# Kernel optimization log

Hardware: AMD Instinct MI355X
Metric: run time of the kernel (lower is better)

The kernel has to match this reference:

```python
import jax, jax.numpy as jnp
from jax import lax
import numpy as np

T, N, C, D, K = 256, 4096, 12, 256, 12


def setup_inputs() -> dict:
    key = jax.random.key(0)
    ks = jax.random.split(key, 11)
    g = lambda k, shape: (jax.random.normal(k, shape, jnp.float32) * 0.05)
    return {
        "x": jax.random.normal(ks[0], (T, N, C), jnp.float32),
        "enc_Wx": g(ks[1], (D, C)),
        "enc_bx": g(ks[2], (D,)),
        "enc_Wh": g(ks[3], (D, D)),
        "enc_Wy": g(ks[4], (K, D)),
        "enc_by": g(ks[5], (K,)),
        "dec_Wx": g(ks[6], (D, C)),
        "dec_bx": g(ks[7], (D,)),
        "dec_Wh": g(ks[8], (D, D)),
        "dec_Wy": g(ks[9], (K, D)),
        "dec_by": g(ks[10], (K,)),
    }


def reference(x, enc_Wx, enc_bx, enc_Wh, enc_Wy, enc_by,
              dec_Wx, dec_bx, dec_Wh, dec_Wy, dec_by):
    # x: (T, N, C)
    Tn, Nn, Cn = x.shape
    Dn = enc_Wh.shape[0]

    # ---- encoder Elman RNN: h_t = relu(x2h(x_t) + h2h(h_{t-1})) ----
    # Precompute input projection for all timesteps (batched GEMM),
    # leaving only the D x D recurrence inside the scan.
    x_proj = jnp.einsum('tnc,dc->tnd', x, enc_Wx) + enc_bx  # (T, N, D)

    def enc_step(h, xp):
        h = jax.nn.relu(xp + h @ enc_Wh.T)
        return h, None

    h0 = jnp.zeros((Nn, Dn), x.dtype)
    h_last, _ = lax.scan(enc_step, h0, x_proj)  # (N, D) == enc_h[-1]
    # (encoder h2y output is computed in the original but discarded)

    # ---- decoder: greedy feedback loop, T steps ----
    sos0 = jnp.zeros((Nn, Cn), x.dtype).at[:, -2].set(1.0)

    def dec_step(carry, _):
        h, sos = carry
        h = jax.nn.relu(sos @ dec_Wx.T + dec_bx + h @ dec_Wh.T)  # (N, D)
        y = h @ dec_Wy.T + dec_by                                # (N, K)
        sos = jax.nn.one_hot(jnp.argmax(y, axis=-1), y.shape[-1],
                             dtype=x.dtype)                      # (N, C)
        return (h, sos), y

    _, ys = lax.scan(dec_step, (h_last, sos0), None, length=Tn)
    return ys  # (T, N, K)
```

## Files before the change

### kernel.cpp

```cpp
#include <hip/hip_runtime.h>
#include <cstdint>
#include <cstddef>

#define TT 256
#define NN 4096
#define CC 12
#define DD 256
#define KD 12
#define NB 16
#define NTH 512
#define HS 264
#define XS 40

typedef _Float16 half8 __attribute__((ext_vector_type(8)));
typedef float f32x4 __attribute__((ext_vector_type(4)));
#define MFMA __builtin_amdgcn_mfma_f32_16x16x32_f16

struct FalseC { static constexpr bool value = false; };
struct TrueC  { static constexpr bool value = true;  };

struct alignas(16) SM {
  _Float16 hhi[2][NB][HS];
  _Float16 hlo[2][NB][HS];
  _Float16 xhi[4][NB][XS];
  _Float16 xlo[4][NB][XS];
  float    part[8][64][4];
  int      idxbuf[16];
};

__device__ __forceinline__ void split8(const float* w, half8& hi, half8& lo) {
  #pragma unroll
  for (int j = 0; j < 8; ++j) {
    _Float16 h = (_Float16)w[j];
    hi[j] = h;
    lo[j] = (_Float16)(w[j] - (float)h);
  }
}

__device__ __forceinline__ void BAR() {
  asm volatile("s_waitcnt lgkmcnt(0)" ::: "memory");
  __builtin_amdgcn_s_barrier();
  __builtin_amdgcn_sched_barrier(0);
}

__global__ __launch_bounds__(NTH, 2)
void seq2seq_kernel(const float* __restrict__ x,
                    const float* __restrict__ enc_Wx,
                    const float* __restrict__ enc_bx,
                    const float* __restrict__ enc_Wh,
                    const float* __restrict__ dec_Wx,
                    const float* __restrict__ dec_bx,
                    const float* __restrict__ dec_Wh,
                    const float* __restrict__ dec_Wy,
                    const float* __restrict__ dec_by,
                    float* __restrict__ out)
{
  __shared__ SM sm;
  const int tid  = (int)threadIdx.x;
  const int wid  = tid >> 6;
  const int lane = tid & 63;
  const int l15  = lane & 15;
  const int quad = lane >> 4;
  const int n0   = (int)blockIdx.x * NB;

  half8 Whi[2][8], Wlo[2][8];
  half8 Xhi[2], Xlo[2];
  float bxr[2];
  float pfA0 = 0.f, pfA1 = 0.f, pfA2 = 0.f;
  float pfB0 = 0.f, pfB1 = 0.f, pfB2 = 0.f;

  if (wid == 1) {
    const float* xg = x + ((size_t)1 * NN + n0) * CC;
    pfB0 = xg[lane]; pfB1 = xg[lane + 64]; pfB2 = xg[lane + 128];
  }

  auto loadWh = [&](const float* __restrict__ W) {
    #pragma unroll
    for (int tt = 0; tt < 2; ++tt) {
      const int n = (wid * 2 + tt) * 16 + l15;
      #pragma unroll
      for (int c = 0; c < 8; ++c) {
        float w[8];
        const float* p = W + (size_t)n * DD + c * 32 + quad * 8;
        *(float4*)&w[0] = *(const float4*)p;
        *(float4*)&w[4] = *(const float4*)(p + 4);
        split8(w, Whi[tt][c], Wlo[tt][c]);
      }
    }
  };
  auto loadWx = [&](const float* __restrict__ Wx) {
    #pragma unroll
    for (int tt = 0; tt < 2; ++tt) {
      const int n = (wid * 2 + tt) * 16 + l15;
      float w[8];
      #pragma unroll
      for (int j = 0; j < 8; ++j) {
        const int k = quad * 8 + j;
        w[j] = (k < CC) ? Wx[(size_t)n * CC + k] : 0.f;
      }
      split8(w, Xhi[tt], Xlo[tt]);
    }
  };
  auto loadBx = [&](const float* __restrict__ bx) {
    #pragma unroll
    for (int tt = 0; tt < 2; ++tt) bxr[tt] = bx[(wid * 2 + tt) * 16 + l15];
  };

  {
    unsigned* z;
    z = (unsigned*)&sm.hhi[0][0][0];
    for (int i = tid; i < NB * HS / 2; i += NTH) z[i] = 0u;
    z = (unsigned*)&sm.hlo[0][0][0];
    for (int i = tid; i < NB * HS / 2; i += NTH) z[i] = 0u;
    z = (unsigned*)&sm.xhi[0][0][0];
    for (int i = tid; i < 4 * NB * XS / 2; i += NTH) z[i] = 0u;
    z = (unsigned*)&sm.xlo[0][0][0];
    for (int i = tid; i < 4 * NB * XS / 2; i += NTH) z[i] = 0u;
  }
  loadWh(enc_Wh);
  loadWx(enc_Wx);
  loadBx(enc_bx);
  BAR();
  if (tid < NB * CC) {
    const float v = x[(size_t)n0 * CC + tid];
    const _Float16 h = (_Float16)v;
    sm.xhi[0][tid / CC][tid % CC] = h;
    sm.xlo[0][tid / CC][tid % CC] = (_Float16)(v - (float)h);
  }
  BAR();

  auto encStep = [&](int t, auto IAc) {
    constexpr bool IA = decltype(IAc)::value;
    if (wid == 1) {
      const int tp = (t + 2 < TT) ? (t + 2) : (TT - 1);
      const float* xg = x + ((size_t)tp * NN + n0) * CC;
      if constexpr (IA) { pfA0 = xg[lane]; pfA1 = xg[lane + 64]; pfA2 = xg[lane + 128]; }
      else              { pfB0 = xg[lane]; pfB1 = xg[lane + 64]; pfB2 = xg[lane + 128]; }
    }
    const int rb = t & 1, wb = rb ^ 1, xs = t & 3;
    f32x4 aA0 = {0.f,0.f,0.f,0.f}, aA1 = {0.f,0.f,0.f,0.f};
    f32x4 aB0 = {0.f,0.f,0.f,0.f}, aB1 = {0.f,0.f,0.f,0.f};
    const half8 xh = *(const half8*)&sm.xhi[xs][l15][quad * 8];
    const half8 xl = *(const half8*)&sm.xlo[xs][l15][quad * 8];
    aA0 = MFMA(xh, Xhi[0], aA0, 0, 0, 0);
    aA1 = MFMA(xh, Xhi[1], aA1, 0, 0, 0);
    aB0 = MFMA(xl, Xhi[0], aB0, 0, 0, 0);
    aB1 = MFMA(xl, Xhi[1], aB1, 0, 0, 0);
    aB0 = MFMA(xh, Xlo[0], aB0, 0, 0, 0);
    aB1 = MFMA(xh, Xlo[1], aB1, 0, 0, 0);
    const _Float16* hh = &sm.hhi[rb][l15][0];
    const _Float16* hl = &sm.hlo[rb][l15][0];
    #pragma unroll
    for (int c = 0; c < 8; ++c) {
      const half8 ahi = *(const half8*)(hh + c * 32 + quad * 8);
      const half8 alo = *(const half8*)(hl + c * 32 + quad * 8);
      aA0 = MFMA(ahi, Whi[0][c], aA0, 0, 0, 0);
      aA1 = MFMA(ahi, Whi[1][c], aA1, 0, 0, 0);
      aB0 = MFMA(alo, Whi[0][c], aB0, 0, 0, 0);
      aB1 = MFMA(alo, Whi[1][c], aB1, 0, 0, 0);
      aA0 = MFMA(ahi, Wlo[0][c], aA0, 0, 0, 0);
      aA1 = MFMA(ahi, Wlo[1][c], aA1, 0, 0, 0);
    }
    #pragma unroll
    for (int r = 0; r < 4; ++r) {
      const int m = quad * 4 + r;
      const float v0 = fmaxf(aA0[r] + aB0[r] + bxr[0], 0.f);
      const float v1 = fmaxf(aA1[r] + aB1[r] + bxr[1], 0.f);
      const _Float16 h0 = (_Float16)v0, h1 = (_Float16)v1;
      sm.hhi[wb][m][(wid * 2 + 0) * 16 + l15] = h0;
      sm.hlo[wb][m][(wid * 2 + 0) * 16 + l15] = (_Float16)(v0 - (float)h0);
      sm.hhi[wb][m][(wid * 2 + 1) * 16 + l15] = h1;
      sm.hlo[wb][m][(wid * 2 + 1) * 16 + l15] = (_Float16)(v1 - (float)h1);
    }
    if (wid == 1) {
      const int xw = (t + 1) & 3;
      float w0, w1, w2;
      if constexpr (IA) { w0 = pfB0; w1 = pfB1; w2 = pfB2; }
      else              { w0 = pfA0; w1 = pfA1; w2 = pfA2; }
      #pragma unroll
      for (int j = 0; j < 3; ++j) {
        const int i = lane + 64 * j;
        const float vv = (j == 0) ? w0 : (j == 1) ? w1 : w2;
        const _Float16 hx = (_Float16)vv;
        sm.xhi[xw][i / CC][i % CC] = hx;
        sm.xlo[xw][i / CC][i % CC] = (_Float16)(vv - (float)hx);
      }
    }
    BAR();
  };

  for (int t = 0; t < TT; t += 2) {
    encStep(t, TrueC{});
    encStep(t + 1, FalseC{});
  }

  loadWh(dec_Wh);
  loadWx(dec_Wx);
  loadBx(dec_bx);
  const float byv = (l15 < KD) ? dec_by[l15] : 0.f;
  half8 wyh, wyl;
  {
    float w[8];
    if (l15 < KD) {
      const float* p = dec_Wy + (size_t)l15 * DD + wid * 32 + quad * 8;
      *(float4*)&w[0] = *(const float4*)p;
      *(float4*)&w[4] = *(const float4*)(p + 4);
    } else {
      #pragma unroll
      for (int j = 0; j < 8; ++j) w[j] = 0.f;
    }
    split8(w, wyh, wyl);
  }
  half8 aX;
  #pragma unroll
  for (int j = 0; j < 8; ++j)
    aX[j] = (_Float16)((quad * 8 + j == CC - 2) ? 1.f : 0.f);

  for (int t = 0; t < TT; ++t) {
    const int rb = t & 1, wb = rb ^ 1;
    f32x4 aA0 = {0.f,0.f,0.f,0.f}, aA1 = {0.f,0.f,0.f,0.f};
    f32x4 aB0 = {0.f,0.f,0.f,0.f}, aB1 = {0.f,0.f,0.f,0.f};
    aA0 = MFMA(aX, Xhi[0], aA0, 0, 0, 0);
    aA1 = MFMA(aX, Xhi[1], aA1, 0, 0, 0);
    aB0 = MFMA(aX, Xlo[0], aB0, 0, 0, 0);
    aB1 = MFMA(aX, Xlo[1], aB1, 0, 0, 0);
    const _Float16* hh = &sm.hhi[rb][l15][0];
    const _Float16* hl = &sm.hlo[rb][l15][0];
    #pragma unroll
    for (int c = 0; c < 8; ++c) {
      const half8 ahi = *(const half8*)(hh + c * 32 + quad * 8);
      const half8 alo = *(const half8*)(hl + c * 32 + quad * 8);
      aA0 = MFMA(ahi, Whi[0][c], aA0, 0, 0, 0);
      aA1 = MFMA(ahi, Whi[1][c], aA1, 0, 0, 0);
      aB0 = MFMA(alo, Whi[0][c], aB0, 0, 0, 0);
      aB1 = MFMA(alo, Whi[1][c], aB1, 0, 0, 0);
      aA0 = MFMA(ahi, Wlo[0][c], aA0, 0, 0, 0);
      aA1 = MFMA(ahi, Wlo[1][c], aA1, 0, 0, 0);
    }
    #pragma unroll
    for (int r = 0; r < 4; ++r) {
      const int m = quad * 4 + r;
      const float v0 = fmaxf(aA0[r] + aB0[r] + bxr[0], 0.f);
      const float v1 = fmaxf(aA1[r] + aB1[r] + bxr[1], 0.f);
      const _Float16 h0 = (_Float16)v0, h1 = (_Float16)v1;
      sm.hhi[wb][m][(wid * 2 + 0) * 16 + l15] = h0;
      sm.hlo[wb][m][(wid * 2 + 0) * 16 + l15] = (_Float16)(v0 - (float)h0);
      sm.hhi[wb][m][(wid * 2 + 1) * 16 + l15] = h1;
      sm.hlo[wb][m][(wid * 2 + 1) * 16 + l15] = (_Float16)(v1 - (float)h1);
    }
    asm volatile("s_waitcnt lgkmcnt(0)" ::: "memory");
    const half8 yh8 = *(const half8*)&sm.hhi[wb][l15][wid * 32 + quad * 8];
    const half8 yl8 = *(const half8*)&sm.hlo[wb][l15][wid * 32 + quad * 8];
    f32x4 yp = {0.f,0.f,0.f,0.f};
    yp = MFMA(yh8, wyh, yp, 0, 0, 0);
    yp = MFMA(yl8, wyh, yp, 0, 0, 0);
    yp = MFMA(yh8, wyl, yp, 0, 0, 0);
    *(f32x4*)&sm.part[wid][lane][0] = yp;
    BAR();
    const int o  = l15;
    const int rl = (lane >> 4) & 1;
    const int sh = lane >> 5;
    const int m  = 2 * wid + rl;
    const int mq = m >> 2, mr = m & 3;
    const int pl = mq * 16 + o;
    float s0 = sm.part[4 * sh + 0][pl][mr] + sm.part[4 * sh + 1][pl][mr]
             + sm.part[4 * sh + 2][pl][mr] + sm.part[4 * sh + 3][pl][mr];
    s0 += __shfl_xor(s0, 32);
    const float yv = s0 + byv;
    if (sh == 0 && o < KD)
      out[((size_t)t * NN + n0 + m) * KD + o] = yv;
    float v = (o < KD) ? yv : -1e30f;
    int io = o;
    #pragma unroll
    for (int d = 1; d < 16; d <<= 1) {
      const float ov = __shfl_xor(v, d);
      const int   oi = __shfl_xor(io, d);
      const bool take = (ov > v) || (ov == v && oi < io);
      v  = take ? ov : v;
      io = take ? oi : io;
    }
    if (sh == 0 && o == 0) sm.idxbuf[m] = io;
    BAR();
    const int g = sm.idxbuf[l15];
    #pragma unroll
    for (int j = 0; j < 8; ++j)
      aX[j] = (_Float16)((quad * 8 + j == g) ? 1.f : 0.f);
  }
}

extern "C" void kernel_launch(void* const* d_in, const int* in_sizes, int n_in,
                              void* d_out, int out_size, void* d_ws, size_t ws_size,
                              hipStream_t stream) {
  (void)in_sizes; (void)n_in; (void)d_ws; (void)ws_size; (void)out_size;
  const float* x      = (const float*)d_in[0];
  const float* enc_Wx = (const float*)d_in[1];
  const float* enc_bx = (const float*)d_in[2];
  const float* enc_Wh = (const float*)d_in[3];
  const float* dec_Wx = (const float*)d_in[6];
  const float* dec_bx = (const float*)d_in[7];
  const float* dec_Wh = (const float*)d_in[8];
  const float* dec_Wy = (const float*)d_in[9];
  const float* dec_by = (const float*)d_in[10];
  float* outp = (float*)d_out;

  seq2seq_kernel<<<NN / NB, NTH, 0, stream>>>(
      x, enc_Wx, enc_bx, enc_Wh, dec_Wx, dec_bx, dec_Wh, dec_Wy, dec_by, outp);
}
```

Before: 871.8 us.

## Reduce decoder output via LDS atomics and drop second per-step barrier

Each wave now adds its partial output-projection MFMA result into a triple-buffered LDS array with atomicAdd, instead of writing per-wave partials that are summed afterwards. Every wave then reads the full 16x12 logits and computes the argmax redundantly, which removes the index buffer and the second barrier in each decoder step. Hidden-state columns are remapped so each lane writes two adjacent fp16 values as one packed 32-bit store, and the barrier helper drops the scheduling barrier. The cost is LDS atomic traffic, redundant argmax work in every wave, and a rotating zeroing of the third reduction buffer.

```diff
diff --git a/kernel.cpp b/kernel.cpp
--- a/kernel.cpp
+++ b/kernel.cpp
@@ -11,6 +11,7 @@
 #define NTH 512
 #define HS 264
 #define XS 40
+#define YS 20
 
 typedef _Float16 half8 __attribute__((ext_vector_type(8)));
 typedef float f32x4 __attribute__((ext_vector_type(4)));
@@ -24,8 +25,7 @@
   _Float16 hlo[2][NB][HS];
   _Float16 xhi[4][NB][XS];
   _Float16 xlo[4][NB][XS];
-  float    part[8][64][4];
-  int      idxbuf[16];
+  float    yred[3][NB][YS];
 };
 
 __device__ __forceinline__ void split8(const float* w, half8& hi, half8& lo) {
@@ -37,10 +37,14 @@
   }
 }
 
+__device__ __forceinline__ unsigned pack2(_Float16 a, _Float16 b) {
+  union { _Float16 h[2]; unsigned u; } x;
+  x.h[0] = a; x.h[1] = b;
+  return x.u;
+}
+
 __device__ __forceinline__ void BAR() {
-  asm volatile("s_waitcnt lgkmcnt(0)" ::: "memory");
-  __builtin_amdgcn_s_barrier();
-  __builtin_amdgcn_sched_barrier(0);
+  asm volatile("s_waitcnt lgkmcnt(0)\n\ts_barrier" ::: "memory");
 }
 
 __global__ __launch_bounds__(NTH, 2)
@@ -77,7 +81,7 @@
   auto loadWh = [&](const float* __restrict__ W) {
     #pragma unroll
     for (int tt = 0; tt < 2; ++tt) {
-      const int n = (wid * 2 + tt) * 16 + l15;
+      const int n = wid * 32 + 2 * l15 + tt;
       #pragma unroll
       for (int c = 0; c < 8; ++c) {
         float w[8];
@@ -91,7 +95,7 @@
   auto loadWx = [&](const float* __restrict__ Wx) {
     #pragma unroll
     for (int tt = 0; tt < 2; ++tt) {
-      const int n = (wid * 2 + tt) * 16 + l15;
+      const int n = wid * 32 + 2 * l15 + tt;
       float w[8];
       #pragma unroll
       for (int j = 0; j < 8; ++j) {
@@ -103,7 +107,7 @@
   };
   auto loadBx = [&](const float* __restrict__ bx) {
     #pragma unroll
-    for (int tt = 0; tt < 2; ++tt) bxr[tt] = bx[(wid * 2 + tt) * 16 + l15];
+    for (int tt = 0; tt < 2; ++tt) bxr[tt] = bx[wid * 32 + 2 * l15 + tt];
   };
 
   {
@@ -161,16 +165,16 @@
       aA0 = MFMA(ahi, Wlo[0][c], aA0, 0, 0, 0);
       aA1 = MFMA(ahi, Wlo[1][c], aA1, 0, 0, 0);
     }
+    const int colh = wid * 32 + 2 * l15;
     #pragma unroll
     for (int r = 0; r < 4; ++r) {
       const int m = quad * 4 + r;
       const float v0 = fmaxf(aA0[r] + aB0[r] + bxr[0], 0.f);
       const float v1 = fmaxf(aA1[r] + aB1[r] + bxr[1], 0.f);
       const _Float16 h0 = (_Float16)v0, h1 = (_Float16)v1;
-      sm.hhi[wb][m][(wid * 2 + 0) * 16 + l15] = h0;
-      sm.hlo[wb][m][(wid * 2 + 0) * 16 + l15] = (_Float16)(v0 - (float)h0);
-      sm.hhi[wb][m][(wid * 2 + 1) * 16 + l15] = h1;
-      sm.hlo[wb][m][(wid * 2 + 1) * 16 + l15] = (_Float16)(v1 - (float)h1);
+      *(unsigned*)&sm.hhi[wb][m][colh] = pack2(h0, h1);
+      *(unsigned*)&sm.hlo[wb][m][colh] =
+          pack2((_Float16)(v0 - (float)h0), (_Float16)(v1 - (float)h1));
     }
     if (wid == 1) {
       const int xw = (t + 1) & 3;
@@ -197,7 +201,12 @@
   loadWh(dec_Wh);
   loadWx(dec_Wx);
   loadBx(dec_bx);
-  const float byv = (l15 < KD) ? dec_by[l15] : 0.f;
+  float by4[4];
+  #pragma unroll
+  for (int j = 0; j < 4; ++j) {
+    const int o = quad * 4 + j;
+    by4[j] = (o < KD) ? dec_by[o] : 0.f;
+  }
   half8 wyh, wyl;
   {
     float w[8];
@@ -215,9 +224,15 @@
   #pragma unroll
   for (int j = 0; j < 8; ++j)
     aX[j] = (_Float16)((quad * 8 + j == CC - 2) ? 1.f : 0.f);
+  {
+    float* zp = &sm.yred[0][0][0];
+    for (int i = tid; i < 3 * NB * YS; i += NTH) zp[i] = 0.f;
+  }
+  BAR();
 
   for (int t = 0; t < TT; ++t) {
     const int rb = t & 1, wb = rb ^ 1;
+    const int yb = t % 3, zb = (t + 2) % 3;
     f32x4 aA0 = {0.f,0.f,0.f,0.f}, aA1 = {0.f,0.f,0.f,0.f};
     f32x4 aB0 = {0.f,0.f,0.f,0.f}, aB1 = {0.f,0.f,0.f,0.f};
     aA0 = MFMA(aX, Xhi[0], aA0, 0, 0, 0);
@@ -237,16 +252,16 @@
       aA0 = MFMA(ahi, Wlo[0][c], aA0, 0, 0, 0);
       aA1 = MFMA(ahi, Wlo[1][c], aA1, 0, 0, 0);
     }
+    const int colh = wid * 32 + 2 * l15;
     #pragma unroll
     for (int r = 0; r < 4; ++r) {
       const int m = quad * 4 + r;
       const float v0 = fmaxf(aA0[r] + aB0[r] + bxr[0], 0.f);
       const float v1 = fmaxf(aA1[r] + aB1[r] + bxr[1], 0.f);
       const _Float16 h0 = (_Float16)v0, h1 = (_Float16)v1;
-      sm.hhi[wb][m][(wid * 2 + 0) * 16 + l15] = h0;
-      sm.hlo[wb][m][(wid * 2 + 0) * 16 + l15] = (_Float16)(v0 - (float)h0);
-      sm.hhi[wb][m][(wid * 2 + 1) * 16 + l15] = h1;
-      sm.hlo[wb][m][(wid * 2 + 1) * 16 + l15] = (_Float16)(v1 - (float)h1);
+      *(unsigned*)&sm.hhi[wb][m][colh] = pack2(h0, h1);
+      *(unsigned*)&sm.hlo[wb][m][colh] =
+          pack2((_Float16)(v0 - (float)h0), (_Float16)(v1 - (float)h1));
     }
     asm volatile("s_waitcnt lgkmcnt(0)" ::: "memory");
     const half8 yh8 = *(const half8*)&sm.hhi[wb][l15][wid * 32 + quad * 8];
@@ -255,36 +270,42 @@
     yp = MFMA(yh8, wyh, yp, 0, 0, 0);
     yp = MFMA(yl8, wyh, yp, 0, 0, 0);
     yp = MFMA(yh8, wyl, yp, 0, 0, 0);
-    *(f32x4*)&sm.part[wid][lane][0] = yp;
+    #pragma unroll
+    for (int r = 0; r < 4; ++r)
+      atomicAdd(&sm.yred[yb][quad * 4 + r][l15], yp[r]);
     BAR();
-    const int o  = l15;
-    const int rl = (lane >> 4) & 1;
-    const int sh = lane >> 5;
-    const int m  = 2 * wid + rl;
-    const int mq = m >> 2, mr = m & 3;
-    const int pl = mq * 16 + o;
-    float s0 = sm.part[4 * sh + 0][pl][mr] + sm.part[4 * sh + 1][pl][mr]
-             + sm.part[4 * sh + 2][pl][mr] + sm.part[4 * sh + 3][pl][mr];
-    s0 += __shfl_xor(s0, 32);
-    const float yv = s0 + byv;
-    if (sh == 0 && o < KD)
-      out[((size_t)t * NN + n0 + m) * KD + o] = yv;
-    float v = (o < KD) ? yv : -1e30f;
-    int io = o;
-    #pragma unroll
-    for (int d = 1; d < 16; d <<= 1) {
+    const f32x4 y4 = *(const f32x4*)&sm.yred[yb][l15][quad * 4];
+    float yv[4];
+    #pragma unroll
+    for (int j = 0; j < 4; ++j) yv[j] = y4[j] + by4[j];
+    if (wid == 0 && quad < 3) {
+      float4 st; st.x = yv[0]; st.y = yv[1]; st.z = yv[2]; st.w = yv[3];
+      *(float4*)&out[((size_t)t * NN + n0 + l15) * KD + quad * 4] = st;
+    }
+    float v = -1e30f; int io = 0;
+    #pragma unroll
+    for (int j = 0; j < 4; ++j) {
+      const int o = quad * 4 + j;
+      const float cv = (o < KD) ? yv[j] : -1e30f;
+      const bool take = cv > v;
+      io = take ? o : io;
+      v  = take ? cv : v;
+    }
+    #pragma unroll
+    for (int d = 16; d < 64; d <<= 1) {
       const float ov = __shfl_xor(v, d);
       const int   oi = __shfl_xor(io, d);
       const bool take = (ov > v) || (ov == v && oi < io);
       v  = take ? ov : v;
       io = take ? oi : io;
     }
-    if (sh == 0 && o == 0) sm.idxbuf[m] = io;
-    BAR();
-    const int g = sm.idxbuf[l15];
     #pragma unroll
     for (int j = 0; j < 8; ++j)
-      aX[j] = (_Float16)((quad * 8 + j == g) ? 1.f : 0.f);
+      aX[j] = (_Float16)((quad * 8 + j == io) ? 1.f : 0.f);
+    {
+      float* zp = &sm.yred[zb][0][0];
+      if (tid < NB * YS) zp[tid] = 0.f;
+    }
   }
 }
 
```

Measured after the change: 1.395 ms. 1.6x slower.
